# Kernel optimization log

Hardware: AMD Instinct MI355X
Metric: run time of the kernel (lower is better)

Reference implementation:

```python
import jax, jax.numpy as jnp
import numpy as np

V = 128          # vocab_size
S = 32           # sentence_size
E = 16           # embedding_size
M = 128          # memory_size
L = 128          # linear_output_size
B = 16
N = 127


def _position_encoding(sentence_size, embedding_size):
    enc = np.ones((embedding_size, sentence_size), dtype=np.float32)
    ls = sentence_size + 1
    le = embedding_size + 1
    for i in range(1, le):
        for j in range(1, ls):
            enc[i - 1, j - 1] = (i - (le - 1) / 2) * (j - (ls - 1) / 2)
    enc = 1 + 4 * enc / embedding_size / sentence_size
    return enc.T  # [S, E]


def setup_inputs() -> dict:
    key = jax.random.key(0)
    ks = jax.random.split(key, 12)
    node_fts = jax.random.randint(ks[0], (B, N, S), 0, V).astype(jnp.float32)
    edge_fts = jax.random.randint(ks[1], (B, N, N, S), 0, V).astype(jnp.float32)
    graph_fts = jax.random.randint(ks[2], (B, S), 0, V).astype(jnp.float32)
    adj_mat = jax.random.randint(ks[3], (B, N, N), 0, 2).astype(jnp.float32)
    hidden = jnp.zeros((B, N, E), jnp.float32)
    sc = 0.02
    query_biases = sc * jax.random.normal(ks[4], (V - 1, E), jnp.float32)
    stories_biases = sc * jax.random.normal(ks[5], (V - 1, E), jnp.float32)
    output_biases = sc * jax.random.normal(ks[6], (V - 1, E), jnp.float32)
    memory_contents = sc * jax.random.normal(ks[7], (M, E), jnp.float32)
    W_int = sc * jax.random.normal(ks[8], (E, E), jnp.float32)   # intermediate_linear (unused, num_hops=1)
    W_out = sc * jax.random.normal(ks[9], (E, L), jnp.float32)   # output_linear
    W_fin = sc * jax.random.normal(ks[10], (L, V), jnp.float32)  # final_linear
    enc = jnp.asarray(_position_encoding(S, E))
    return dict(node_fts=node_fts, edge_fts=edge_fts, graph_fts=graph_fts,
                adj_mat=adj_mat, hidden=hidden, enc=enc,
                query_biases=query_biases, stories_biases=stories_biases,
                output_biases=output_biases, memory_contents=memory_contents,
                W_int=W_int, W_out=W_out, W_fin=W_fin)


def reference(node_fts, edge_fts, graph_fts, adj_mat, hidden, enc,
              query_biases, stories_biases, output_biases, memory_contents,
              W_int, W_out, W_fin):
    del hidden
    b, n, s = node_fts.shape
    # [B, N+1, S]: nodes plus graph feature row
    naf = jnp.concatenate([node_fts, graph_fts[:, None, :]], axis=1)
    # mask edges then pad to [B, N+1, N+1, S]
    ef = edge_fts * adj_mat[..., None]
    ef = jnp.pad(ef, ((0, 0), (0, 1), (0, 1), (0, 0)))
    bt = b * (n + 1)
    queries = naf.reshape(bt, s)                 # [BT, S]
    stories = ef.reshape(bt, n + 1, s)           # [BT, M0, S], M0 = N+1

    nil = jnp.zeros((1, enc.shape[1]), queries.dtype)
    sb = jnp.concatenate([stories_biases, nil], axis=0)   # [V, E]
    qb = jnp.concatenate([query_biases, nil], axis=0)
    ob = jnp.concatenate([output_biases, nil], axis=0)

    sidx = jnp.maximum(stories.astype(jnp.int32), 0)       # clamp_min(0)
    qidx = jnp.maximum(queries.astype(jnp.int32), 0)

    # position-encoded weighted sums over the sentence axis
    mem = jnp.einsum('bmse,se->bme', sb[sidx], enc)        # [BT, M0, E]
    Cj = jnp.einsum('bmse,se->bme', ob[sidx], enc)         # [BT, M0, E]
    pad_m = memory_contents.shape[0] - (n + 1)
    mem = jnp.pad(mem, ((0, 0), (0, pad_m), (0, 0))) + memory_contents
    Cj = jnp.pad(Cj, ((0, 0), (0, pad_m), (0, 0)))
    u = jnp.einsum('bse,se->be', qb[qidx], enc)            # [BT, E]

    # num_hops = 1
    x = u
    probs = jax.nn.softmax(jnp.einsum('bme,be->bm', mem, x), axis=-1)
    o = jnp.einsum('bme,bm->be', Cj, probs)
    x = jax.nn.relu((x + o) @ W_out)                       # last hop -> output_linear + relu
    ret = x @ W_fin                                        # [BT, V]

    nxt = ret.reshape(b, n + 1, -1)
    return nxt[:, :-1, :] + nxt[:, -1:, :]                 # [B, N, V]
```

## Files before the change

kernel.cpp:

```cpp
#include <hip/hip_runtime.h>

#define Vn 128
#define Sn 32
#define En 16
#define M0 128
#define Ln 128
#define Bn 16
#define Nn 127
#define NBLK (Bn * Nn)
#define TRS 36

__global__ __launch_bounds__(256, 5) void memnet_fused(
    const float* __restrict__ node_fts, const float* __restrict__ edge_fts,
    const float* __restrict__ graph_fts, const float* __restrict__ adjm,
    const float* __restrict__ enc, const float* __restrict__ qb,
    const float* __restrict__ sb, const float* __restrict__ ob,
    const float* __restrict__ mc, const float* __restrict__ wout,
    const float* __restrict__ wfin, float* __restrict__ out)
{
    __shared__ __align__(16) float tbl[M0 * TRS];
    __shared__ __align__(16) float encL[Sn * En];
    __shared__ unsigned int idxw[M0 * 8];
    __shared__ float scoresL[M0];
    __shared__ float probsL[M0];
    __shared__ float uL[En];
    __shared__ float ugL[En];
    __shared__ float uoL[En];
    __shared__ float cM[En];
    __shared__ float cC[En];
    __shared__ float xL[Ln];
    __shared__ float xgL[Ln];
    __shared__ float xg2L[Vn];
    __shared__ float owaveL[4 * En];
    __shared__ float red[4], red2[4];
    __shared__ int listL[128];
    __shared__ int flagL[128];
    __shared__ int wcnt[2];

    const int t = threadIdx.x;
    const int bt = blockIdx.x;
    const int b = bt / 127;
    const int lane = t & 63;
    const int wv = t >> 6;

    for (int c = t; c < 1024; c += 256) {
        int r = c >> 3, q = c & 7;
        float4 v = make_float4(0.f, 0.f, 0.f, 0.f);
        if (r < 127)
            v = *(const float4*)((q < 4) ? &sb[r * 16 + q * 4]
                                         : &ob[r * 16 + (q - 4) * 4]);
        *(float4*)&tbl[r * TRS + q * 4] = v;
    }
    if (t < 128) *(float4*)&encL[t * 4] = *(const float4*)&enc[t * 4];

    if (t < 128) {
        bool flag = (t < 127) && (adjm[(size_t)bt * 127 + t] != 0.f);
        unsigned long long msk = __ballot(flag);
        int pos = (int)__popcll(msk & ((1ull << lane) - 1ull));
        if (flag) listL[(t & 64) + pos] = t;
        if (lane == 0) wcnt[t >> 6] = (int)__popcll(msk);
        flagL[t] = flag ? 1 : 0;
    }
    for (int c = t; c < 1024; c += 256) {
        int m = c >> 3, q = c & 7;
        if (m < 127 && adjm[(size_t)bt * 127 + m] != 0.f) {
            float4 v = *(const float4*)&edge_fts[(size_t)(bt * 127 + m) * 32 + q * 4];
            idxw[m * 8 + q] = (unsigned)(int)v.x | ((unsigned)(int)v.y << 8)
                            | ((unsigned)(int)v.z << 16) | ((unsigned)(int)v.w << 24);
        }
    }
    if (lane < 16) {
        if (wv == 0) {
            float ue = 0.f;
            for (int s = 0; s < 32; s++) {
                int qi = (int)node_fts[(size_t)bt * 32 + s];
                if (qi < 0) qi = 0;
                float w = (qi < 127) ? qb[qi * 16 + lane] : 0.f;
                ue = fmaf(w, enc[s * 16 + lane], ue);
            }
            uL[lane] = ue;
        } else if (wv == 1) {
            float es = 0.f;
            for (int s = 0; s < 32; s++) es += enc[s * 16 + lane];
            cM[lane] = sb[lane] * es;
            cC[lane] = ob[lane] * es;
        } else if (wv == 2) {
            float ue = 0.f;
            for (int s = 0; s < 32; s++) {
                int qi = (int)graph_fts[b * 32 + s];
                if (qi < 0) qi = 0;
                float w = (qi < 127) ? qb[qi * 16 + lane] : 0.f;
                ue = fmaf(w, enc[s * 16 + lane], ue);
            }
            ugL[lane] = ue;
        }
    }
    __syncthreads();

    if (t < 128 && !flagL[t]) {
        float p = 0.f;
#pragma unroll
        for (int e4 = 0; e4 < 16; e4 += 4) {
            float4 m4 = *(const float4*)&mc[t * 16 + e4];
            p = fmaf(cM[e4 + 0] + m4.x, uL[e4 + 0], p);
            p = fmaf(cM[e4 + 1] + m4.y, uL[e4 + 1], p);
            p = fmaf(cM[e4 + 2] + m4.z, uL[e4 + 2], p);
            p = fmaf(cM[e4 + 3] + m4.w, uL[e4 + 3], p);
        }
        scoresL[t] = p;
    }

    const int eg4 = (t & 3) * 4;
    const int qd = t >> 2;
    const int c0 = wcnt[0];
    const int nact = c0 + wcnt[1];
    const float4 u4 = *(const float4*)&uL[eg4];

    float4 aC_A = make_float4(0.f, 0.f, 0.f, 0.f);
    float4 aC_B = make_float4(0.f, 0.f, 0.f, 0.f);
    int mA = -1, mB = -1;

    if (qd < nact) {
        mA = listL[(qd < c0) ? qd : (qd - c0 + 64)];
        float4 aM = make_float4(0.f, 0.f, 0.f, 0.f);
        for (int sq = 0; sq < 8; sq++) {
            unsigned w0 = idxw[mA * 8 + sq];
#pragma unroll
            for (int j = 0; j < 4; j++) {
                int s = sq * 4 + j;
                int i0 = (w0 >> (8 * j)) & 0xFF;
                float4 eb = *(const float4*)&encL[s * 16 + eg4];
                const float* rp = &tbl[i0 * TRS + eg4];
                float4 a0 = *(const float4*)rp;
                float4 c0v = *(const float4*)(rp + 16);
                aM.x = fmaf(a0.x, eb.x, aM.x); aM.y = fmaf(a0.y, eb.y, aM.y);
                aM.z = fmaf(a0.z, eb.z, aM.z); aM.w = fmaf(a0.w, eb.w, aM.w);
                aC_A.x = fmaf(c0v.x, eb.x, aC_A.x); aC_A.y = fmaf(c0v.y, eb.y, aC_A.y);
                aC_A.z = fmaf(c0v.z, eb.z, aC_A.z); aC_A.w = fmaf(c0v.w, eb.w, aC_A.w);
            }
        }
        float4 mc4 = *(const float4*)&mc[mA * 16 + eg4];
        float p = (aM.x + mc4.x) * u4.x + (aM.y + mc4.y) * u4.y
                + (aM.z + mc4.z) * u4.z + (aM.w + mc4.w) * u4.w;
        p += __shfl_xor(p, 1); p += __shfl_xor(p, 2);
        if ((t & 3) == 0) scoresL[mA] = p;
    }
    if (qd + 64 < nact) {
        int g = qd + 64;
        mB = listL[(g < c0) ? g : (g - c0 + 64)];
        float4 aM = make_float4(0.f, 0.f, 0.f, 0.f);
        for (int sq = 0; sq < 8; sq++) {
            unsigned w0 = idxw[mB * 8 + sq];
#pragma unroll
            for (int j = 0; j < 4; j++) {
                int s = sq * 4 + j;
                int i0 = (w0 >> (8 * j)) & 0xFF;
                float4 eb = *(const float4*)&encL[s * 16 + eg4];
                const float* rp = &tbl[i0 * TRS + eg4];
                float4 a0 = *(const float4*)rp;
                float4 c0v = *(const float4*)(rp + 16);
                aM.x = fmaf(a0.x, eb.x, aM.x); aM.y = fmaf(a0.y, eb.y, aM.y);
                aM.z = fmaf(a0.z, eb.z, aM.z); aM.w = fmaf(a0.w, eb.w, aM.w);
                aC_B.x = fmaf(c0v.x, eb.x, aC_B.x); aC_B.y = fmaf(c0v.y, eb.y, aC_B.y);
                aC_B.z = fmaf(c0v.z, eb.z, aC_B.z); aC_B.w = fmaf(c0v.w, eb.w, aC_B.w);
            }
        }
        float4 mc4 = *(const float4*)&mc[mB * 16 + eg4];
        float p = (aM.x + mc4.x) * u4.x + (aM.y + mc4.y) * u4.y
                + (aM.z + mc4.z) * u4.z + (aM.w + mc4.w) * u4.w;
        p += __shfl_xor(p, 1); p += __shfl_xor(p, 2);
        if ((t & 3) == 0) scoresL[mB] = p;
    }
    __syncthreads();

    float pmask;
    {
        float v = (t < 128) ? scoresL[t] : -1e30f;
#pragma unroll
        for (int off = 32; off > 0; off >>= 1) v = fmaxf(v, __shfl_xor(v, off));
        if (lane == 0) red[wv] = v;
        __syncthreads();
        float mx = fmaxf(fmaxf(red[0], red[1]), fmaxf(red[2], red[3]));
        float ex = (t < 128) ? __expf(scoresL[t] - mx) : 0.f;
        float exm = (t < 128 && !flagL[t]) ? ex : 0.f;
        float sv = ex, sm = exm;
#pragma unroll
        for (int off = 32; off > 0; off >>= 1) {
            sv += __shfl_xor(sv, off);
            sm += __shfl_xor(sm, off);
        }
        __syncthreads();
        if (lane == 0) { red[wv] = sv; red2[wv] = sm; }
        __syncthreads();
        float sum = red[0] + red[1] + red[2] + red[3];
        pmask = (red2[0] + red2[1] + red2[2] + red2[3]) / sum;
        if (t < 128) probsL[t] = ex / sum;
    }
    __syncthreads();

    {
        float4 op = make_float4(0.f, 0.f, 0.f, 0.f);
        if (mA >= 0) {
            float pa = probsL[mA];
            op.x = pa * aC_A.x; op.y = pa * aC_A.y;
            op.z = pa * aC_A.z; op.w = pa * aC_A.w;
        }
        if (mB >= 0) {
            float pb = probsL[mB];
            op.x = fmaf(pb, aC_B.x, op.x); op.y = fmaf(pb, aC_B.y, op.y);
            op.z = fmaf(pb, aC_B.z, op.z); op.w = fmaf(pb, aC_B.w, op.w);
        }
#pragma unroll
        for (int off = 4; off <= 32; off <<= 1) {
            op.x += __shfl_xor(op.x, off);
            op.y += __shfl_xor(op.y, off);
            op.z += __shfl_xor(op.z, off);
            op.w += __shfl_xor(op.w, off);
        }
        if (lane < 4) *(float4*)&owaveL[wv * 16 + lane * 4] = op;
    }
    __syncthreads();
    if (t < 16) {
        float o = owaveL[t] + owaveL[16 + t] + owaveL[32 + t] + owaveL[48 + t];
        uoL[t] = uL[t] + o + cC[t] * pmask;
    }
    __syncthreads();

    if (t < 128) {
        float acc = 0.f;
#pragma unroll
        for (int e = 0; e < 16; e++) acc = fmaf(uoL[e], wout[e * 128 + t], acc);
        xL[t] = fmaxf(acc, 0.f);
    } else {
        int l = t - 128;
        float acc = 0.f;
#pragma unroll
        for (int e = 0; e < 16; e++) acc = fmaf(ugL[e] + cC[e], wout[e * 128 + l], acc);
        xgL[l] = fmaxf(acc, 0.f);
    }
    __syncthreads();

    {
        const int vcol = t & 127;
        const float* xsrc = (t < 128) ? xL : xgL;
        float acc = 0.f;
        for (int l = 0; l < 128; l++) acc = fmaf(xsrc[l], wfin[l * 128 + vcol], acc);
        if (t >= 128) xg2L[vcol] = acc;
        __syncthreads();
        if (t < 128) out[(size_t)bt * 128 + vcol] = acc + xg2L[vcol];
    }
}

extern "C" void kernel_launch(void* const* d_in, const int* in_sizes, int n_in,
                              void* d_out, int out_size, void* d_ws, size_t ws_size,
                              hipStream_t stream)
{
    const float* node  = (const float*)d_in[0];
    const float* edge  = (const float*)d_in[1];
    const float* graph = (const float*)d_in[2];
    const float* adjm  = (const float*)d_in[3];
    const float* enc   = (const float*)d_in[5];
    const float* qb    = (const float*)d_in[6];
    const float* sb    = (const float*)d_in[7];
    const float* ob    = (const float*)d_in[8];
    const float* mc    = (const float*)d_in[9];
    const float* wout  = (const float*)d_in[11];
    const float* wfin  = (const float*)d_in[12];

    memnet_fused<<<NBLK, 256, 0, stream>>>(node, edge, graph, adjm, enc, qb,
                                           sb, ob, mc, wout, wfin, (float*)d_out);
}
```

Baseline: 132.6 us.

## Process two rows per block and load edge indices via registers and shuffles

Each block now handles two consecutive (batch,node) rows, so the shared bias table, encoding and constant setup are loaded once per two rows. This halves the grid and the per-block setup cost. The shared idxw staging of edge-feature indices is removed: each quad of threads loads its edge row directly, packs the indices into registers and broadcasts them with __shfl, which frees shared memory and drops a pass and a barrier. In exchange, launch bounds drop to 4 blocks per CU and the two rows run one after the other, with extra barriers inside each block.

New measurement: 395.5 us. 2.98x slower.

```diff
diff --git a/kernel.cpp b/kernel.cpp
--- a/kernel.cpp
+++ b/kernel.cpp
@@ -7,10 +7,11 @@
 #define Ln 128
 #define Bn 16
 #define Nn 127
-#define NBLK (Bn * Nn)
+#define NROWS (Bn * Nn)
+#define NBLK (NROWS / 2)
 #define TRS 36
 
-__global__ __launch_bounds__(256, 5) void memnet_fused(
+__global__ __launch_bounds__(256, 4) void memnet_fused(
     const float* __restrict__ node_fts, const float* __restrict__ edge_fts,
     const float* __restrict__ graph_fts, const float* __restrict__ adjm,
     const float* __restrict__ enc, const float* __restrict__ qb,
@@ -20,7 +21,6 @@
 {
     __shared__ __align__(16) float tbl[M0 * TRS];
     __shared__ __align__(16) float encL[Sn * En];
-    __shared__ unsigned int idxw[M0 * 8];
     __shared__ float scoresL[M0];
     __shared__ float probsL[M0];
     __shared__ float uL[En];
@@ -38,8 +38,6 @@
     __shared__ int wcnt[2];
 
     const int t = threadIdx.x;
-    const int bt = blockIdx.x;
-    const int b = bt / 127;
     const int lane = t & 63;
     const int wv = t >> 6;
 
@@ -52,202 +50,216 @@
         *(float4*)&tbl[r * TRS + q * 4] = v;
     }
     if (t < 128) *(float4*)&encL[t * 4] = *(const float4*)&enc[t * 4];
-
-    if (t < 128) {
-        bool flag = (t < 127) && (adjm[(size_t)bt * 127 + t] != 0.f);
-        unsigned long long msk = __ballot(flag);
-        int pos = (int)__popcll(msk & ((1ull << lane) - 1ull));
-        if (flag) listL[(t & 64) + pos] = t;
-        if (lane == 0) wcnt[t >> 6] = (int)__popcll(msk);
-        flagL[t] = flag ? 1 : 0;
+    if (wv == 1 && lane < 16) {
+        float es = 0.f;
+        for (int s = 0; s < 32; s++) es += enc[s * 16 + lane];
+        cM[lane] = sb[lane] * es;
+        cC[lane] = ob[lane] * es;
     }
-    for (int c = t; c < 1024; c += 256) {
-        int m = c >> 3, q = c & 7;
-        if (m < 127 && adjm[(size_t)bt * 127 + m] != 0.f) {
-            float4 v = *(const float4*)&edge_fts[(size_t)(bt * 127 + m) * 32 + q * 4];
-            idxw[m * 8 + q] = (unsigned)(int)v.x | ((unsigned)(int)v.y << 8)
-                            | ((unsigned)(int)v.z << 16) | ((unsigned)(int)v.w << 24);
-        }
-    }
-    if (lane < 16) {
-        if (wv == 0) {
-            float ue = 0.f;
-            for (int s = 0; s < 32; s++) {
-                int qi = (int)node_fts[(size_t)bt * 32 + s];
-                if (qi < 0) qi = 0;
-                float w = (qi < 127) ? qb[qi * 16 + lane] : 0.f;
-                ue = fmaf(w, enc[s * 16 + lane], ue);
-            }
-            uL[lane] = ue;
-        } else if (wv == 1) {
-            float es = 0.f;
-            for (int s = 0; s < 32; s++) es += enc[s * 16 + lane];
-            cM[lane] = sb[lane] * es;
-            cC[lane] = ob[lane] * es;
-        } else if (wv == 2) {
-            float ue = 0.f;
-            for (int s = 0; s < 32; s++) {
-                int qi = (int)graph_fts[b * 32 + s];
-                if (qi < 0) qi = 0;
-                float w = (qi < 127) ? qb[qi * 16 + lane] : 0.f;
-                ue = fmaf(w, enc[s * 16 + lane], ue);
-            }
-            ugL[lane] = ue;
-        }
-    }
-    __syncthreads();
-
-    if (t < 128 && !flagL[t]) {
-        float p = 0.f;
-#pragma unroll
-        for (int e4 = 0; e4 < 16; e4 += 4) {
-            float4 m4 = *(const float4*)&mc[t * 16 + e4];
-            p = fmaf(cM[e4 + 0] + m4.x, uL[e4 + 0], p);
-            p = fmaf(cM[e4 + 1] + m4.y, uL[e4 + 1], p);
-            p = fmaf(cM[e4 + 2] + m4.z, uL[e4 + 2], p);
-            p = fmaf(cM[e4 + 3] + m4.w, uL[e4 + 3], p);
-        }
-        scoresL[t] = p;
-    }
-
-    const int eg4 = (t & 3) * 4;
-    const int qd = t >> 2;
-    const int c0 = wcnt[0];
-    const int nact = c0 + wcnt[1];
-    const float4 u4 = *(const float4*)&uL[eg4];
-
-    float4 aC_A = make_float4(0.f, 0.f, 0.f, 0.f);
-    float4 aC_B = make_float4(0.f, 0.f, 0.f, 0.f);
-    int mA = -1, mB = -1;
-
-    if (qd < nact) {
-        mA = listL[(qd < c0) ? qd : (qd - c0 + 64)];
-        float4 aM = make_float4(0.f, 0.f, 0.f, 0.f);
-        for (int sq = 0; sq < 8; sq++) {
-            unsigned w0 = idxw[mA * 8 + sq];
-#pragma unroll
-            for (int j = 0; j < 4; j++) {
-                int s = sq * 4 + j;
-                int i0 = (w0 >> (8 * j)) & 0xFF;
-                float4 eb = *(const float4*)&encL[s * 16 + eg4];
-                const float* rp = &tbl[i0 * TRS + eg4];
-                float4 a0 = *(const float4*)rp;
-                float4 c0v = *(const float4*)(rp + 16);
-                aM.x = fmaf(a0.x, eb.x, aM.x); aM.y = fmaf(a0.y, eb.y, aM.y);
-                aM.z = fmaf(a0.z, eb.z, aM.z); aM.w = fmaf(a0.w, eb.w, aM.w);
-                aC_A.x = fmaf(c0v.x, eb.x, aC_A.x); aC_A.y = fmaf(c0v.y, eb.y, aC_A.y);
-                aC_A.z = fmaf(c0v.z, eb.z, aC_A.z); aC_A.w = fmaf(c0v.w, eb.w, aC_A.w);
-            }
-        }
-        float4 mc4 = *(const float4*)&mc[mA * 16 + eg4];
-        float p = (aM.x + mc4.x) * u4.x + (aM.y + mc4.y) * u4.y
-                + (aM.z + mc4.z) * u4.z + (aM.w + mc4.w) * u4.w;
-        p += __shfl_xor(p, 1); p += __shfl_xor(p, 2);
-        if ((t & 3) == 0) scoresL[mA] = p;
-    }
-    if (qd + 64 < nact) {
-        int g = qd + 64;
-        mB = listL[(g < c0) ? g : (g - c0 + 64)];
-        float4 aM = make_float4(0.f, 0.f, 0.f, 0.f);
-        for (int sq = 0; sq < 8; sq++) {
-            unsigned w0 = idxw[mB * 8 + sq];
-#pragma unroll
-            for (int j = 0; j < 4; j++) {
-                int s = sq * 4 + j;
-                int i0 = (w0 >> (8 * j)) & 0xFF;
-                float4 eb = *(const float4*)&encL[s * 16 + eg4];
-                const float* rp = &tbl[i0 * TRS + eg4];
-                float4 a0 = *(const float4*)rp;
-                float4 c0v = *(const float4*)(rp + 16);
-                aM.x = fmaf(a0.x, eb.x, aM.x); aM.y = fmaf(a0.y, eb.y, aM.y);
-                aM.z = fmaf(a0.z, eb.z, aM.z); aM.w = fmaf(a0.w, eb.w, aM.w);
-                aC_B.x = fmaf(c0v.x, eb.x, aC_B.x); aC_B.y = fmaf(c0v.y, eb.y, aC_B.y);
-                aC_B.z = fmaf(c0v.z, eb.z, aC_B.z); aC_B.w = fmaf(c0v.w, eb.w, aC_B.w);
-            }
-        }
-        float4 mc4 = *(const float4*)&mc[mB * 16 + eg4];
-        float p = (aM.x + mc4.x) * u4.x + (aM.y + mc4.y) * u4.y
-                + (aM.z + mc4.z) * u4.z + (aM.w + mc4.w) * u4.w;
-        p += __shfl_xor(p, 1); p += __shfl_xor(p, 2);
-        if ((t & 3) == 0) scoresL[mB] = p;
-    }
-    __syncthreads();
-
-    float pmask;
-    {
-        float v = (t < 128) ? scoresL[t] : -1e30f;
-#pragma unroll
-        for (int off = 32; off > 0; off >>= 1) v = fmaxf(v, __shfl_xor(v, off));
-        if (lane == 0) red[wv] = v;
-        __syncthreads();
-        float mx = fmaxf(fmaxf(red[0], red[1]), fmaxf(red[2], red[3]));
-        float ex = (t < 128) ? __expf(scoresL[t] - mx) : 0.f;
-        float exm = (t < 128 && !flagL[t]) ? ex : 0.f;
-        float sv = ex, sm = exm;
-#pragma unroll
-        for (int off = 32; off > 0; off >>= 1) {
-            sv += __shfl_xor(sv, off);
-            sm += __shfl_xor(sm, off);
-        }
-        __syncthreads();
-        if (lane == 0) { red[wv] = sv; red2[wv] = sm; }
-        __syncthreads();
-        float sum = red[0] + red[1] + red[2] + red[3];
-        pmask = (red2[0] + red2[1] + red2[2] + red2[3]) / sum;
-        if (t < 128) probsL[t] = ex / sum;
-    }
-    __syncthreads();
-
-    {
-        float4 op = make_float4(0.f, 0.f, 0.f, 0.f);
-        if (mA >= 0) {
-            float pa = probsL[mA];
-            op.x = pa * aC_A.x; op.y = pa * aC_A.y;
-            op.z = pa * aC_A.z; op.w = pa * aC_A.w;
-        }
-        if (mB >= 0) {
-            float pb = probsL[mB];
-            op.x = fmaf(pb, aC_B.x, op.x); op.y = fmaf(pb, aC_B.y, op.y);
-            op.z = fmaf(pb, aC_B.z, op.z); op.w = fmaf(pb, aC_B.w, op.w);
-        }
-#pragma unroll
-        for (int off = 4; off <= 32; off <<= 1) {
-            op.x += __shfl_xor(op.x, off);
-            op.y += __shfl_xor(op.y, off);
-            op.z += __shfl_xor(op.z, off);
-            op.w += __shfl_xor(op.w, off);
-        }
-        if (lane < 4) *(float4*)&owaveL[wv * 16 + lane * 4] = op;
-    }
-    __syncthreads();
-    if (t < 16) {
-        float o = owaveL[t] + owaveL[16 + t] + owaveL[32 + t] + owaveL[48 + t];
-        uoL[t] = uL[t] + o + cC[t] * pmask;
-    }
-    __syncthreads();
-
-    if (t < 128) {
-        float acc = 0.f;
-#pragma unroll
-        for (int e = 0; e < 16; e++) acc = fmaf(uoL[e], wout[e * 128 + t], acc);
-        xL[t] = fmaxf(acc, 0.f);
-    } else {
-        int l = t - 128;
-        float acc = 0.f;
-#pragma unroll
-        for (int e = 0; e < 16; e++) acc = fmaf(ugL[e] + cC[e], wout[e * 128 + l], acc);
-        xgL[l] = fmaxf(acc, 0.f);
-    }
-    __syncthreads();
-
-    {
-        const int vcol = t & 127;
-        const float* xsrc = (t < 128) ? xL : xgL;
-        float acc = 0.f;
-        for (int l = 0; l < 128; l++) acc = fmaf(xsrc[l], wfin[l * 128 + vcol], acc);
-        if (t >= 128) xg2L[vcol] = acc;
-        __syncthreads();
-        if (t < 128) out[(size_t)bt * 128 + vcol] = acc + xg2L[vcol];
+
+    for (int rr = 0; rr < 2; rr++) {
+        const int bt = blockIdx.x * 2 + rr;
+        const int b = bt / 127;
+
+        if (t < 128) {
+            bool flag = (t < 127) && (adjm[(size_t)bt * 127 + t] != 0.f);
+            unsigned long long msk = __ballot(flag);
+            int pos = (int)__popcll(msk & ((1ull << lane) - 1ull));
+            if (flag) listL[(t & 64) + pos] = t;
+            if (lane == 0) wcnt[t >> 6] = (int)__popcll(msk);
+            flagL[t] = flag ? 1 : 0;
+        }
+        if (lane < 16) {
+            if (wv == 0) {
+                float ue = 0.f;
+                for (int s = 0; s < 32; s++) {
+                    int qi = (int)node_fts[(size_t)bt * 32 + s];
+                    if (qi < 0) qi = 0;
+                    float w = (qi < 127) ? qb[qi * 16 + lane] : 0.f;
+                    ue = fmaf(w, enc[s * 16 + lane], ue);
+                }
+                uL[lane] = ue;
+            } else if (wv == 2) {
+                float ue = 0.f;
+                for (int s = 0; s < 32; s++) {
+                    int qi = (int)graph_fts[b * 32 + s];
+                    if (qi < 0) qi = 0;
+                    float w = (qi < 127) ? qb[qi * 16 + lane] : 0.f;
+                    ue = fmaf(w, enc[s * 16 + lane], ue);
+                }
+                ugL[lane] = ue;
+            }
+        }
+        __syncthreads();
+
+        if (t < 128 && !flagL[t]) {
+            float p = 0.f;
+#pragma unroll
+            for (int e4 = 0; e4 < 16; e4 += 4) {
+                float4 m4 = *(const float4*)&mc[t * 16 + e4];
+                p = fmaf(cM[e4 + 0] + m4.x, uL[e4 + 0], p);
+                p = fmaf(cM[e4 + 1] + m4.y, uL[e4 + 1], p);
+                p = fmaf(cM[e4 + 2] + m4.z, uL[e4 + 2], p);
+                p = fmaf(cM[e4 + 3] + m4.w, uL[e4 + 3], p);
+            }
+            scoresL[t] = p;
+        }
+
+        const int eg4 = (t & 3) * 4;
+        const int qd = t >> 2;
+        const int qbase = lane & ~3;
+        const int c0 = wcnt[0];
+        const int nact = c0 + wcnt[1];
+        const float4 u4 = *(const float4*)&uL[eg4];
+
+        float4 aC_A = make_float4(0.f, 0.f, 0.f, 0.f);
+        float4 aC_B = make_float4(0.f, 0.f, 0.f, 0.f);
+        int mA = -1, mB = -1;
+
+        if (qd < nact) {
+            mA = listL[(qd < c0) ? qd : (qd - c0 + 64)];
+            const float* er = &edge_fts[(size_t)(bt * 127 + mA) * 32];
+            float4 fa = *(const float4*)&er[(t & 3) * 4];
+            float4 fb = *(const float4*)&er[16 + (t & 3) * 4];
+            unsigned pk0 = (unsigned)(int)fa.x | ((unsigned)(int)fa.y << 8)
+                         | ((unsigned)(int)fa.z << 16) | ((unsigned)(int)fa.w << 24);
+            unsigned pk1 = (unsigned)(int)fb.x | ((unsigned)(int)fb.y << 8)
+                         | ((unsigned)(int)fb.z << 16) | ((unsigned)(int)fb.w << 24);
+            float4 aM = make_float4(0.f, 0.f, 0.f, 0.f);
+            for (int sq = 0; sq < 8; sq++) {
+                unsigned w0 = __shfl((sq < 4) ? pk0 : pk1, qbase + (sq & 3));
+#pragma unroll
+                for (int j = 0; j < 4; j++) {
+                    int s = sq * 4 + j;
+                    int i0 = (w0 >> (8 * j)) & 0xFF;
+                    float4 eb = *(const float4*)&encL[s * 16 + eg4];
+                    const float* rp = &tbl[i0 * TRS + eg4];
+                    float4 a0 = *(const float4*)rp;
+                    float4 c0v = *(const float4*)(rp + 16);
+                    aM.x = fmaf(a0.x, eb.x, aM.x); aM.y = fmaf(a0.y, eb.y, aM.y);
+                    aM.z = fmaf(a0.z, eb.z, aM.z); aM.w = fmaf(a0.w, eb.w, aM.w);
+                    aC_A.x = fmaf(c0v.x, eb.x, aC_A.x); aC_A.y = fmaf(c0v.y, eb.y, aC_A.y);
+                    aC_A.z = fmaf(c0v.z, eb.z, aC_A.z); aC_A.w = fmaf(c0v.w, eb.w, aC_A.w);
+                }
+            }
+            float4 mc4 = *(const float4*)&mc[mA * 16 + eg4];
+            float p = (aM.x + mc4.x) * u4.x + (aM.y + mc4.y) * u4.y
+                    + (aM.z + mc4.z) * u4.z + (aM.w + mc4.w) * u4.w;
+            p += __shfl_xor(p, 1); p += __shfl_xor(p, 2);
+            if ((t & 3) == 0) scoresL[mA] = p;
+        }
+        if (qd + 64 < nact) {
+            int g = qd + 64;
+            mB = listL[(g < c0) ? g : (g - c0 + 64)];
+            const float* er = &edge_fts[(size_t)(bt * 127 + mB) * 32];
+            float4 fa = *(const float4*)&er[(t & 3) * 4];
+            float4 fb = *(const float4*)&er[16 + (t & 3) * 4];
+            unsigned pk0 = (unsigned)(int)fa.x | ((unsigned)(int)fa.y << 8)
+                         | ((unsigned)(int)fa.z << 16) | ((unsigned)(int)fa.w << 24);
+            unsigned pk1 = (unsigned)(int)fb.x | ((unsigned)(int)fb.y << 8)
+                         | ((unsigned)(int)fb.z << 16) | ((unsigned)(int)fb.w << 24);
+            float4 aM = make_float4(0.f, 0.f, 0.f, 0.f);
+            for (int sq = 0; sq < 8; sq++) {
+                unsigned w0 = __shfl((sq < 4) ? pk0 : pk1, qbase + (sq & 3));
+#pragma unroll
+                for (int j = 0; j < 4; j++) {
+                    int s = sq * 4 + j;
+                    int i0 = (w0 >> (8 * j)) & 0xFF;
+                    float4 eb = *(const float4*)&encL[s * 16 + eg4];
+                    const float* rp = &tbl[i0 * TRS + eg4];
+                    float4 a0 = *(const float4*)rp;
+                    float4 c0v = *(const float4*)(rp + 16);
+                    aM.x = fmaf(a0.x, eb.x, aM.x); aM.y = fmaf(a0.y, eb.y, aM.y);
+                    aM.z = fmaf(a0.z, eb.z, aM.z); aM.w = fmaf(a0.w, eb.w, aM.w);
+                    aC_B.x = fmaf(c0v.x, eb.x, aC_B.x); aC_B.y = fmaf(c0v.y, eb.y, aC_B.y);
+                    aC_B.z = fmaf(c0v.z, eb.z, aC_B.z); aC_B.w = fmaf(c0v.w, eb.w, aC_B.w);
+                }
+            }
+            float4 mc4 = *(const float4*)&mc[mB * 16 + eg4];
+            float p = (aM.x + mc4.x) * u4.x + (aM.y + mc4.y) * u4.y
+                    + (aM.z + mc4.z) * u4.z + (aM.w + mc4.w) * u4.w;
+            p += __shfl_xor(p, 1); p += __shfl_xor(p, 2);
+            if ((t & 3) == 0) scoresL[mB] = p;
+        }
+        __syncthreads();
+
+        float pmask;
+        {
+            float v = (t < 128) ? scoresL[t] : -1e30f;
+#pragma unroll
+            for (int off = 32; off > 0; off >>= 1) v = fmaxf(v, __shfl_xor(v, off));
+            if (lane == 0) red[wv] = v;
+            __syncthreads();
+            float mx = fmaxf(fmaxf(red[0], red[1]), fmaxf(red[2], red[3]));
+            float ex = (t < 128) ? __expf(scoresL[t] - mx) : 0.f;
+            float exm = (t < 128 && !flagL[t]) ? ex : 0.f;
+            float sv = ex, sm = exm;
+#pragma unroll
+            for (int off = 32; off > 0; off >>= 1) {
+                sv += __shfl_xor(sv, off);
+                sm += __shfl_xor(sm, off);
+            }
+            __syncthreads();
+            if (lane == 0) { red[wv] = sv; red2[wv] = sm; }
+            __syncthreads();
+            float sum = red[0] + red[1] + red[2] + red[3];
+            pmask = (red2[0] + red2[1] + red2[2] + red2[3]) / sum;
+            if (t < 128) probsL[t] = ex / sum;
+        }
+        __syncthreads();
+
+        {
+            float4 op = make_float4(0.f, 0.f, 0.f, 0.f);
+            if (mA >= 0) {
+                float pa = probsL[mA];
+                op.x = pa * aC_A.x; op.y = pa * aC_A.y;
+                op.z = pa * aC_A.z; op.w = pa * aC_A.w;
+            }
+            if (mB >= 0) {
+                float pb = probsL[mB];
+                op.x = fmaf(pb, aC_B.x, op.x); op.y = fmaf(pb, aC_B.y, op.y);
+                op.z = fmaf(pb, aC_B.z, op.z); op.w = fmaf(pb, aC_B.w, op.w);
+            }
+#pragma unroll
+            for (int off = 4; off <= 32; off <<= 1) {
+                op.x += __shfl_xor(op.x, off);
+                op.y += __shfl_xor(op.y, off);
+                op.z += __shfl_xor(op.z, off);
+                op.w += __shfl_xor(op.w, off);
+            }
+            if (lane < 4) *(float4*)&owaveL[wv * 16 + lane * 4] = op;
+        }
+        __syncthreads();
+        if (t < 16) {
+            float o = owaveL[t] + owaveL[16 + t] + owaveL[32 + t] + owaveL[48 + t];
+            uoL[t] = uL[t] + o + cC[t] * pmask;
+        }
+        __syncthreads();
+
+        if (t < 128) {
+            float acc = 0.f;
+#pragma unroll
+            for (int e = 0; e < 16; e++) acc = fmaf(uoL[e], wout[e * 128 + t], acc);
+            xL[t] = fmaxf(acc, 0.f);
+        } else {
+            int l = t - 128;
+            float acc = 0.f;
+#pragma unroll
+            for (int e = 0; e < 16; e++) acc = fmaf(ugL[e] + cC[e], wout[e * 128 + l], acc);
+            xgL[l] = fmaxf(acc, 0.f);
+        }
+        __syncthreads();
+
+        {
+            const int vcol = t & 127;
+            const float* xsrc = (t < 128) ? xL : xgL;
+            float acc = 0.f;
+            for (int l = 0; l < 128; l++) acc = fmaf(xsrc[l], wfin[l * 128 + vcol], acc);
+            if (t >= 128) xg2L[vcol] = acc;
+            __syncthreads();
+            if (t < 128) out[(size_t)bt * 128 + vcol] = acc + xg2L[vcol];
+        }
+        __syncthreads();
     }
 }
 
```

## Process two rows per block to share the staged embedding table

Applied to the files above, without the earlier changes.

Each 512-thread block now handles two (batch,node) rows, one per 256-thread half, and launches half as many blocks. The shared sb/ob table, encoding and constant bias terms are loaded once per block and serve both rows, which halves the per-row staging traffic and setup. Per-row scratch arrays are duplicated in shared memory, which lowers how many blocks fit per CU, and the block-wide barriers now couple the two halves. Launch bounds change to 512 threads with 8 blocks per multiprocessor.

Measured after the change: 136.0 us. 2.5% more time.

```diff
diff --git a/kernel.cpp b/kernel.cpp
--- a/kernel.cpp
+++ b/kernel.cpp
@@ -7,10 +7,11 @@
 #define Ln 128
 #define Bn 16
 #define Nn 127
-#define NBLK (Bn * Nn)
+#define NROWS (Bn * Nn)
+#define NBLK (NROWS / 2)
 #define TRS 36
 
-__global__ __launch_bounds__(256, 5) void memnet_fused(
+__global__ __launch_bounds__(512, 8) void memnet_fused(
     const float* __restrict__ node_fts, const float* __restrict__ edge_fts,
     const float* __restrict__ graph_fts, const float* __restrict__ adjm,
     const float* __restrict__ enc, const float* __restrict__ qb,
@@ -20,30 +21,34 @@
 {
     __shared__ __align__(16) float tbl[M0 * TRS];
     __shared__ __align__(16) float encL[Sn * En];
-    __shared__ unsigned int idxw[M0 * 8];
-    __shared__ float scoresL[M0];
-    __shared__ float probsL[M0];
-    __shared__ float uL[En];
-    __shared__ float ugL[En];
-    __shared__ float uoL[En];
+    __shared__ unsigned int idxw[2][M0 * 8];
+    __shared__ float scoresL[2][M0];
+    __shared__ float probsL[2][M0];
+    __shared__ float uL[2][En];
+    __shared__ float ugL[2][En];
+    __shared__ float uoL[2][En];
     __shared__ float cM[En];
     __shared__ float cC[En];
-    __shared__ float xL[Ln];
-    __shared__ float xgL[Ln];
-    __shared__ float xg2L[Vn];
-    __shared__ float owaveL[4 * En];
-    __shared__ float red[4], red2[4];
-    __shared__ int listL[128];
-    __shared__ int flagL[128];
-    __shared__ int wcnt[2];
+    __shared__ float xL[2][Ln];
+    __shared__ float xgL[2][Ln];
+    __shared__ float xg2L[2][Vn];
+    __shared__ float owaveL[8 * En];
+    __shared__ float red[8], red2[8];
+    __shared__ int listL[2][128];
+    __shared__ int flagL[2][128];
+    __shared__ int wcnt[2][2];
 
     const int t = threadIdx.x;
-    const int bt = blockIdx.x;
-    const int b = bt / 127;
+    const int h = t >> 8;
+    const int ht = t & 255;
     const int lane = t & 63;
     const int wv = t >> 6;
-
-    for (int c = t; c < 1024; c += 256) {
+    const int wl = wv & 3;
+
+    const int bt = blockIdx.x * 2 + h;
+    const int b = bt / 127;
+
+    for (int c = t; c < 1024; c += 512) {
         int r = c >> 3, q = c & 7;
         float4 v = make_float4(0.f, 0.f, 0.f, 0.f);
         if (r < 127)
@@ -53,24 +58,25 @@
     }
     if (t < 128) *(float4*)&encL[t * 4] = *(const float4*)&enc[t * 4];
 
-    if (t < 128) {
-        bool flag = (t < 127) && (adjm[(size_t)bt * 127 + t] != 0.f);
+    if (ht < 128) {
+        bool flag = (ht < 127) && (adjm[(size_t)bt * 127 + ht] != 0.f);
         unsigned long long msk = __ballot(flag);
         int pos = (int)__popcll(msk & ((1ull << lane) - 1ull));
-        if (flag) listL[(t & 64) + pos] = t;
-        if (lane == 0) wcnt[t >> 6] = (int)__popcll(msk);
-        flagL[t] = flag ? 1 : 0;
-    }
-    for (int c = t; c < 1024; c += 256) {
-        int m = c >> 3, q = c & 7;
-        if (m < 127 && adjm[(size_t)bt * 127 + m] != 0.f) {
-            float4 v = *(const float4*)&edge_fts[(size_t)(bt * 127 + m) * 32 + q * 4];
-            idxw[m * 8 + q] = (unsigned)(int)v.x | ((unsigned)(int)v.y << 8)
-                            | ((unsigned)(int)v.z << 16) | ((unsigned)(int)v.w << 24);
+        if (flag) listL[h][(ht & 64) + pos] = ht;
+        if (lane == 0) wcnt[h][ht >> 6] = (int)__popcll(msk);
+        flagL[h][ht] = flag ? 1 : 0;
+    }
+    for (int c = t; c < 2048; c += 512) {
+        int hh = c >> 10, m = (c >> 3) & 127, q = c & 7;
+        int bth = blockIdx.x * 2 + hh;
+        if (m < 127 && adjm[(size_t)bth * 127 + m] != 0.f) {
+            float4 v = *(const float4*)&edge_fts[(size_t)(bth * 127 + m) * 32 + q * 4];
+            idxw[hh][m * 8 + q] = (unsigned)(int)v.x | ((unsigned)(int)v.y << 8)
+                                | ((unsigned)(int)v.z << 16) | ((unsigned)(int)v.w << 24);
         }
     }
     if (lane < 16) {
-        if (wv == 0) {
+        if (wl == 0) {
             float ue = 0.f;
             for (int s = 0; s < 32; s++) {
                 int qi = (int)node_fts[(size_t)bt * 32 + s];
@@ -78,13 +84,8 @@
                 float w = (qi < 127) ? qb[qi * 16 + lane] : 0.f;
                 ue = fmaf(w, enc[s * 16 + lane], ue);
             }
-            uL[lane] = ue;
-        } else if (wv == 1) {
-            float es = 0.f;
-            for (int s = 0; s < 32; s++) es += enc[s * 16 + lane];
-            cM[lane] = sb[lane] * es;
-            cC[lane] = ob[lane] * es;
-        } else if (wv == 2) {
+            uL[h][lane] = ue;
+        } else if (wl == 2) {
             float ue = 0.f;
             for (int s = 0; s < 32; s++) {
                 int qi = (int)graph_fts[b * 32 + s];
@@ -92,39 +93,44 @@
                 float w = (qi < 127) ? qb[qi * 16 + lane] : 0.f;
                 ue = fmaf(w, enc[s * 16 + lane], ue);
             }
-            ugL[lane] = ue;
-        }
-    }
-    __syncthreads();
-
-    if (t < 128 && !flagL[t]) {
+            ugL[h][lane] = ue;
+        } else if (wv == 3) {
+            float es = 0.f;
+            for (int s = 0; s < 32; s++) es += enc[s * 16 + lane];
+            cM[lane] = sb[lane] * es;
+            cC[lane] = ob[lane] * es;
+        }
+    }
+    __syncthreads();
+
+    if (ht < 128 && !flagL[h][ht]) {
         float p = 0.f;
 #pragma unroll
         for (int e4 = 0; e4 < 16; e4 += 4) {
-            float4 m4 = *(const float4*)&mc[t * 16 + e4];
-            p = fmaf(cM[e4 + 0] + m4.x, uL[e4 + 0], p);
-            p = fmaf(cM[e4 + 1] + m4.y, uL[e4 + 1], p);
-            p = fmaf(cM[e4 + 2] + m4.z, uL[e4 + 2], p);
-            p = fmaf(cM[e4 + 3] + m4.w, uL[e4 + 3], p);
-        }
-        scoresL[t] = p;
+            float4 m4 = *(const float4*)&mc[ht * 16 + e4];
+            p = fmaf(cM[e4 + 0] + m4.x, uL[h][e4 + 0], p);
+            p = fmaf(cM[e4 + 1] + m4.y, uL[h][e4 + 1], p);
+            p = fmaf(cM[e4 + 2] + m4.z, uL[h][e4 + 2], p);
+            p = fmaf(cM[e4 + 3] + m4.w, uL[h][e4 + 3], p);
+        }
+        scoresL[h][ht] = p;
     }
 
     const int eg4 = (t & 3) * 4;
-    const int qd = t >> 2;
-    const int c0 = wcnt[0];
-    const int nact = c0 + wcnt[1];
-    const float4 u4 = *(const float4*)&uL[eg4];
+    const int qd = ht >> 2;
+    const int c0 = wcnt[h][0];
+    const int nact = c0 + wcnt[h][1];
+    const float4 u4 = *(const float4*)&uL[h][eg4];
 
     float4 aC_A = make_float4(0.f, 0.f, 0.f, 0.f);
     float4 aC_B = make_float4(0.f, 0.f, 0.f, 0.f);
     int mA = -1, mB = -1;
 
     if (qd < nact) {
-        mA = listL[(qd < c0) ? qd : (qd - c0 + 64)];
+        mA = listL[h][(qd < c0) ? qd : (qd - c0 + 64)];
         float4 aM = make_float4(0.f, 0.f, 0.f, 0.f);
         for (int sq = 0; sq < 8; sq++) {
-            unsigned w0 = idxw[mA * 8 + sq];
+            unsigned w0 = idxw[h][mA * 8 + sq];
 #pragma unroll
             for (int j = 0; j < 4; j++) {
                 int s = sq * 4 + j;
@@ -143,14 +149,14 @@
         float p = (aM.x + mc4.x) * u4.x + (aM.y + mc4.y) * u4.y
                 + (aM.z + mc4.z) * u4.z + (aM.w + mc4.w) * u4.w;
         p += __shfl_xor(p, 1); p += __shfl_xor(p, 2);
-        if ((t & 3) == 0) scoresL[mA] = p;
+        if ((t & 3) == 0) scoresL[h][mA] = p;
     }
     if (qd + 64 < nact) {
         int g = qd + 64;
-        mB = listL[(g < c0) ? g : (g - c0 + 64)];
+        mB = listL[h][(g < c0) ? g : (g - c0 + 64)];
         float4 aM = make_float4(0.f, 0.f, 0.f, 0.f);
         for (int sq = 0; sq < 8; sq++) {
-            unsigned w0 = idxw[mB * 8 + sq];
+            unsigned w0 = idxw[h][mB * 8 + sq];
 #pragma unroll
             for (int j = 0; j < 4; j++) {
                 int s = sq * 4 + j;
@@ -169,20 +175,21 @@
         float p = (aM.x + mc4.x) * u4.x + (aM.y + mc4.y) * u4.y
                 + (aM.z + mc4.z) * u4.z + (aM.w + mc4.w) * u4.w;
         p += __shfl_xor(p, 1); p += __shfl_xor(p, 2);
-        if ((t & 3) == 0) scoresL[mB] = p;
+        if ((t & 3) == 0) scoresL[h][mB] = p;
     }
     __syncthreads();
 
     float pmask;
     {
-        float v = (t < 128) ? scoresL[t] : -1e30f;
+        float v = (ht < 128) ? scoresL[h][ht] : -1e30f;
 #pragma unroll
         for (int off = 32; off > 0; off >>= 1) v = fmaxf(v, __shfl_xor(v, off));
         if (lane == 0) red[wv] = v;
         __syncthreads();
-        float mx = fmaxf(fmaxf(red[0], red[1]), fmaxf(red[2], red[3]));
-        float ex = (t < 128) ? __expf(scoresL[t] - mx) : 0.f;
-        float exm = (t < 128 && !flagL[t]) ? ex : 0.f;
+        float mx = fmaxf(fmaxf(red[h * 4 + 0], red[h * 4 + 1]),
+                         fmaxf(red[h * 4 + 2], red[h * 4 + 3]));
+        float ex = (ht < 128) ? __expf(scoresL[h][ht] - mx) : 0.f;
+        float exm = (ht < 128 && !flagL[h][ht]) ? ex : 0.f;
         float sv = ex, sm = exm;
 #pragma unroll
         for (int off = 32; off > 0; off >>= 1) {
@@ -192,21 +199,21 @@
         __syncthreads();
         if (lane == 0) { red[wv] = sv; red2[wv] = sm; }
         __syncthreads();
-        float sum = red[0] + red[1] + red[2] + red[3];
-        pmask = (red2[0] + red2[1] + red2[2] + red2[3]) / sum;
-        if (t < 128) probsL[t] = ex / sum;
+        float sum = red[h * 4 + 0] + red[h * 4 + 1] + red[h * 4 + 2] + red[h * 4 + 3];
+        pmask = (red2[h * 4 + 0] + red2[h * 4 + 1] + red2[h * 4 + 2] + red2[h * 4 + 3]) / sum;
+        if (ht < 128) probsL[h][ht] = ex / sum;
     }
     __syncthreads();
 
     {
         float4 op = make_float4(0.f, 0.f, 0.f, 0.f);
         if (mA >= 0) {
-            float pa = probsL[mA];
+            float pa = probsL[h][mA];
             op.x = pa * aC_A.x; op.y = pa * aC_A.y;
             op.z = pa * aC_A.z; op.w = pa * aC_A.w;
         }
         if (mB >= 0) {
-            float pb = probsL[mB];
+            float pb = probsL[h][mB];
             op.x = fmaf(pb, aC_B.x, op.x); op.y = fmaf(pb, aC_B.y, op.y);
             op.z = fmaf(pb, aC_B.z, op.z); op.w = fmaf(pb, aC_B.w, op.w);
         }
@@ -220,34 +227,35 @@
         if (lane < 4) *(float4*)&owaveL[wv * 16 + lane * 4] = op;
     }
     __syncthreads();
-    if (t < 16) {
-        float o = owaveL[t] + owaveL[16 + t] + owaveL[32 + t] + owaveL[48 + t];
-        uoL[t] = uL[t] + o + cC[t] * pmask;
-    }
-    __syncthreads();
-
-    if (t < 128) {
+    if (ht < 16) {
+        float o = owaveL[(h * 4 + 0) * 16 + ht] + owaveL[(h * 4 + 1) * 16 + ht]
+                + owaveL[(h * 4 + 2) * 16 + ht] + owaveL[(h * 4 + 3) * 16 + ht];
+        uoL[h][ht] = uL[h][ht] + o + cC[ht] * pmask;
+    }
+    __syncthreads();
+
+    if (ht < 128) {
         float acc = 0.f;
 #pragma unroll
-        for (int e = 0; e < 16; e++) acc = fmaf(uoL[e], wout[e * 128 + t], acc);
-        xL[t] = fmaxf(acc, 0.f);
+        for (int e = 0; e < 16; e++) acc = fmaf(uoL[h][e], wout[e * 128 + ht], acc);
+        xL[h][ht] = fmaxf(acc, 0.f);
     } else {
-        int l = t - 128;
+        int l = ht - 128;
         float acc = 0.f;
 #pragma unroll
-        for (int e = 0; e < 16; e++) acc = fmaf(ugL[e] + cC[e], wout[e * 128 + l], acc);
-        xgL[l] = fmaxf(acc, 0.f);
+        for (int e = 0; e < 16; e++) acc = fmaf(ugL[h][e] + cC[e], wout[e * 128 + l], acc);
+        xgL[h][l] = fmaxf(acc, 0.f);
     }
     __syncthreads();
 
     {
-        const int vcol = t & 127;
-        const float* xsrc = (t < 128) ? xL : xgL;
+        const int vcol = ht & 127;
+        const float* xsrc = (ht < 128) ? xL[h] : xgL[h];
         float acc = 0.f;
         for (int l = 0; l < 128; l++) acc = fmaf(xsrc[l], wfin[l * 128 + vcol], acc);
-        if (t >= 128) xg2L[vcol] = acc;
-        __syncthreads();
-        if (t < 128) out[(size_t)bt * 128 + vcol] = acc + xg2L[vcol];
+        if (ht >= 128) xg2L[h][vcol] = acc;
+        __syncthreads();
+        if (ht < 128) out[(size_t)bt * 128 + vcol] = acc + xg2L[h][vcol];
     }
 }
 
@@ -267,6 +275,6 @@
     const float* wout  = (const float*)d_in[11];
     const float* wfin  = (const float*)d_in[12];
 
-    memnet_fused<<<NBLK, 256, 0, stream>>>(node, edge, graph, adjm, enc, qb,
+    memnet_fused<<<NBLK, 512, 0, stream>>>(node, edge, graph, adjm, enc, qb,
                                            sb, ob, mc, wout, wfin, (float*)d_out);
 }
```
